# Kernel optimization log

Measured on AMD Instinct MI355X. Metric: run time of the kernel, lower is better.

## Reference

```python
import jax, jax.numpy as jnp
import numpy as np

D_MODEL = 512
H = 8


def setup_inputs() -> dict:
    key = jax.random.key(0)
    ks = jax.random.split(key, 11)
    B, L, D = 8, 1024, D_MODEL
    s = 1.0 / np.sqrt(D)
    return {
        "q": jax.random.normal(ks[0], (B, L, D), jnp.float32),
        "k": jax.random.normal(ks[1], (B, L, D), jnp.float32),
        "v": jax.random.normal(ks[2], (B, L, D), jnp.float32),
        "Wq": jax.random.normal(ks[3], (D, D), jnp.float32) * s,
        "bq": jnp.zeros((D,), jnp.float32),
        "Wk": jax.random.normal(ks[4], (D, D), jnp.float32) * s,
        "bk": jnp.zeros((D,), jnp.float32),
        "Wv": jax.random.normal(ks[5], (D, D), jnp.float32) * s,
        "bv": jnp.zeros((D,), jnp.float32),
        "Wo": jax.random.normal(ks[6], (D, D), jnp.float32) * s,
        "bo": jnp.zeros((D,), jnp.float32),
    }


def _split_heads(x, h):
    B, L, D = x.shape
    return x.reshape(B, L, h, D // h).transpose(0, 2, 1, 3)  # (B,h,L,dk)


def reference(q, k, v, Wq, bq, Wk, bk, Wv, bv, Wo, bo):
    B, L, D = q.shape
    dk = D // H
    qw = q @ Wq + bq
    kw = k @ Wk + bk
    vw = q @ Wv + bv  # faithful to source bug: dense_v applied to q, not v
    qh = _split_heads(qw, H)
    kh = _split_heads(kw, H)
    vh = _split_heads(vw, H)
    scale = jnp.asarray(1.0 / np.sqrt(dk), qh.dtype)
    scores = jnp.einsum("bhqd,bhkd->bhqk", qh, kh) * scale  # (B,h,L,L)
    attn = jax.nn.softmax(scores, axis=-1)
    ctx = jnp.einsum("bhqk,bhkd->bhqd", attn, vh)  # (B,h,L,dk)
    out = ctx.transpose(0, 2, 1, 3).reshape(B, L, D) @ Wo + bo
    return out, attn
```

## Files before the change

### kernel.cpp

```cpp
#include <hip/hip_runtime.h>

typedef unsigned short u16;
typedef __bf16 bf16x8 __attribute__((ext_vector_type(8)));
typedef unsigned short u16x8 __attribute__((ext_vector_type(8)));
typedef unsigned short u16x4 __attribute__((ext_vector_type(4)));
typedef float f32x4 __attribute__((ext_vector_type(4)));

#define MFMA16(a, b, c) __builtin_amdgcn_mfma_f32_16x16x32_bf16(a, b, c, 0, 0, 0)

__device__ __forceinline__ u16 f2bf(float f) {
    union { float f; unsigned u; } v; v.f = f;
    unsigned r = v.u + 0x7fffu + ((v.u >> 16) & 1u);
    return (u16)(r >> 16);
}
__device__ __forceinline__ float bf2f(u16 u) {
    union { unsigned u; float f; } v; v.u = (unsigned)u << 16;
    return v.f;
}
__device__ __forceinline__ u16 bfc(float f) {
    return __builtin_bit_cast(u16, (__bf16)f);
}

typedef __attribute__((address_space(1))) void GAS;
typedef __attribute__((address_space(3))) void LAS;
__device__ __forceinline__ void gload_lds16(const void* g, void* l) {
    __builtin_amdgcn_global_load_lds((GAS*)g, (LAS*)l, 16, 0, 0);
}

__global__ __launch_bounds__(256) void wtrans(const float* Wq, const float* Wk,
                                              const float* Wv, const float* Wo, u16* WT) {
    __shared__ float t[32][33];
    const int z = blockIdx.z;
    const float* W = (z == 0) ? Wq : (z == 1) ? Wk : (z == 2) ? Wv : Wo;
    u16* out = WT + (size_t)z * 512 * 512;
    const int tx = threadIdx.x, ty = threadIdx.y;
    const int k0 = blockIdx.y * 32, n0 = blockIdx.x * 32;
#pragma unroll
    for (int p = 0; p < 4; ++p)
        t[ty + 8 * p][tx] = W[(size_t)(k0 + ty + 8 * p) * 512 + n0 + tx];
    __syncthreads();
#pragma unroll
    for (int p = 0; p < 4; ++p) {
        const int n = n0 + ty + 8 * p;
        out[(size_t)n * 512 + k0 + tx] = f2bf(t[tx][ty + 8 * p]);
    }
}

__global__ __launch_bounds__(256) void qkconv(const float* q, const float* k, u16* qb, u16* kb) {
    const size_t n4 = (size_t)8192 * 512 / 4;
    const size_t stride = (size_t)gridDim.x * 256;
    for (size_t i = (size_t)blockIdx.x * 256 + threadIdx.x; i < 2 * n4; i += stride) {
        const float4 v = (i < n4) ? ((const float4*)q)[i] : ((const float4*)k)[i - n4];
        u16x4 o;
        o[0] = f2bf(v.x); o[1] = f2bf(v.y); o[2] = f2bf(v.z); o[3] = f2bf(v.w);
        if (i < n4) ((u16x4*)qb)[i] = o; else ((u16x4*)kb)[i - n4] = o;
    }
}

__global__ __launch_bounds__(256) void vtrans(const u16* vw, u16* vt) {
    __shared__ u16 t[64][72];
    const int l0 = blockIdx.x * 64, h = blockIdx.y, b = blockIdx.z;
    const int tid = threadIdx.x;
    {
        const int r = tid >> 2, c16 = (tid & 3) * 16;
        const u16* src = vw + (size_t)(b * 1024 + l0 + r) * 512 + h * 64 + c16;
        *(u16x8*)(&t[r][c16])     = *(const u16x8*)(src);
        *(u16x8*)(&t[r][c16 + 8]) = *(const u16x8*)(src + 8);
    }
    __syncthreads();
    {
        const int dk = tid >> 2, lc = (tid & 3) * 16;
        u16x8 a0, a1;
#pragma unroll
        for (int e = 0; e < 8; ++e) { a0[e] = t[lc + e][dk]; a1[e] = t[lc + 8 + e][dk]; }
        u16* dst = vt + ((size_t)(b * 8 + h) * 64 + dk) * 1024 + l0 + lc;
        *(u16x8*)dst       = a0;
        *(u16x8*)(dst + 8) = a1;
    }
}

template <bool C_F32>
__device__ __forceinline__ void gemm_core(const u16* A, const u16* Bt,
                                          const float* bias, void* Cp,
                                          int bm, int bn) {
    __shared__ u16 As[128 * 64];
    __shared__ u16 Bs[128 * 64];
    const int tid  = threadIdx.x;
    const int lane = tid & 63;
    const int w    = tid >> 6;
    const int wm   = (w >> 1) * 64;
    const int wn   = (w & 1) * 64;
    const int col  = lane & 15;
    const int quad = lane >> 4;
    const int srow = lane >> 3;
    const int scol = (lane & 7) * 8;

    f32x4 acc[4][4] = {};

    for (int kt = 0; kt < 512; kt += 64) {
        __syncthreads();
#pragma unroll
        for (int p = 0; p < 4; ++p) {
            const int c  = w * 4 + p;
            const int gr = c * 8 + srow;
            gload_lds16(A  + (size_t)(bm * 128 + gr) * 512 + kt + scol, As + c * 512);
            gload_lds16(Bt + (size_t)(bn * 128 + gr) * 512 + kt + scol, Bs + c * 512);
        }
        __syncthreads();
#pragma unroll
        for (int ks = 0; ks < 2; ++ks) {
            const int k0 = ks * 32 + quad * 8;
            bf16x8 af[4], bfr[4];
#pragma unroll
            for (int i = 0; i < 4; ++i)
                af[i] = __builtin_bit_cast(bf16x8, *(const u16x8*)(As + (wm + i * 16 + col) * 64 + k0));
#pragma unroll
            for (int j = 0; j < 4; ++j)
                bfr[j] = __builtin_bit_cast(bf16x8, *(const u16x8*)(Bs + (wn + j * 16 + col) * 64 + k0));
#pragma unroll
            for (int i = 0; i < 4; ++i)
#pragma unroll
                for (int j = 0; j < 4; ++j)
                    acc[i][j] = MFMA16(af[i], bfr[j], acc[i][j]);
        }
    }
#pragma unroll
    for (int j = 0; j < 4; ++j) {
        const int gn = bn * 128 + wn + j * 16 + col;
        const float bv = bias[gn];
#pragma unroll
        for (int i = 0; i < 4; ++i) {
#pragma unroll
            for (int r = 0; r < 4; ++r) {
                const int gm = bm * 128 + wm + i * 16 + quad * 4 + r;
                const float val = acc[i][j][r] + bv;
                if (C_F32) ((float*)Cp)[(size_t)gm * 512 + gn] = val;
                else       ((u16*)Cp)[(size_t)gm * 512 + gn]   = f2bf(val);
            }
        }
    }
}

__global__ __launch_bounds__(256, 3) void qkv_gemm(const u16* qb, const u16* kb, const u16* WT,
                                                   const float* bq, const float* bk, const float* bv,
                                                   u16* out) {
    const int z = blockIdx.z;
    const u16* A      = (z == 1) ? kb : qb;
    const u16* B      = WT + (size_t)z * 512 * 512;
    const float* bias = (z == 0) ? bq : (z == 1) ? bk : bv;
    u16* C            = out + (size_t)z * 8192 * 512;
    gemm_core<false>(A, B, bias, C, blockIdx.x, blockIdx.y);
}

__global__ __launch_bounds__(256, 3) void out_gemm(const u16* ctx, const u16* WoT,
                                                   const float* bo, float* out) {
    gemm_core<true>(ctx, WoT, bo, out, blockIdx.x, blockIdx.y);
}

__global__ __launch_bounds__(512, 4) void attn_kernel(const u16* qw, const u16* kw, const u16* vt,
                                                      float* attn_out, u16* ctx) {
    __shared__ u16 Ks[128 * 72];
    __shared__ u16 Vs[64 * 136];
    __shared__ u16 Ps[8][16 * 136];

    const int bh  = blockIdx.x;
    const int qt  = blockIdx.y;
    const int b   = bh >> 3, h = bh & 7;
    const int tid = threadIdx.x;
    const int lane = tid & 63, w = tid >> 6;
    const int col = lane & 15, quad = lane >> 4;
    const int wq  = w * 16;
    const float scale = 0.125f;

    const size_t headbase = (size_t)b * (1024 * 512) + (size_t)h * 64;
    const u16* vh = vt + (size_t)bh * (64 * 1024);

    const int krow = tid >> 2, koff = (tid & 3) * 16;
    const int vrow = tid >> 3, voff = (tid & 7) * 16;
    const u16* kbase = kw + headbase + (size_t)krow * 512 + koff;
    const u16* vbase = vh + (size_t)vrow * 1024 + voff;

    bf16x8 qf[2];
    {
        const u16* qp = qw + headbase + (size_t)(qt * 128 + wq + col) * 512 + quad * 8;
        qf[0] = __builtin_bit_cast(bf16x8, *(const u16x8*)qp);
        qf[1] = __builtin_bit_cast(bf16x8, *(const u16x8*)(qp + 32));
    }

    float l_acc = 0.f;

    u16x8 rk0 = *(const u16x8*)kbase;
    u16x8 rk1 = *(const u16x8*)(kbase + 8);
    for (int kt = 0; kt < 8; ++kt) {
        __syncthreads();
        *(u16x8*)(Ks + krow * 72 + koff)     = rk0;
        *(u16x8*)(Ks + krow * 72 + koff + 8) = rk1;
        __syncthreads();
        if (kt < 7) {
            const u16* kp = kbase + (size_t)(kt + 1) * (128 * 512);
            rk0 = *(const u16x8*)kp;
            rk1 = *(const u16x8*)(kp + 8);
        }
        f32x4 s[8] = {};
#pragma unroll
        for (int ks = 0; ks < 2; ++ks) {
            const int k0 = ks * 32 + quad * 8;
#pragma unroll
            for (int j = 0; j < 8; ++j) {
                const bf16x8 kf = __builtin_bit_cast(bf16x8,
                    *(const u16x8*)(Ks + (j * 16 + col) * 72 + k0));
                s[j] = MFMA16(kf, qf[ks], s[j]);
            }
        }
#pragma unroll
        for (int j = 0; j < 8; ++j)
#pragma unroll
            for (int r = 0; r < 4; ++r)
                l_acc += __expf(s[j][r] * scale);
    }

    float rinv;
    {
        float l = l_acc;
        l += __shfl_xor(l, 16); l += __shfl_xor(l, 32);
        rinv = 1.0f / l;
    }

    f32x4 o[4] = {};

    rk0 = *(const u16x8*)kbase;
    rk1 = *(const u16x8*)(kbase + 8);
    u16x8 rv0 = *(const u16x8*)vbase;
    u16x8 rv1 = *(const u16x8*)(vbase + 8);
    for (int kt = 0; kt < 8; ++kt) {
        __syncthreads();
        *(u16x8*)(Ks + krow * 72 + koff)      = rk0;
        *(u16x8*)(Ks + krow * 72 + koff + 8)  = rk1;
        *(u16x8*)(Vs + vrow * 136 + voff)     = rv0;
        *(u16x8*)(Vs + vrow * 136 + voff + 8) = rv1;
        __syncthreads();
        if (kt < 7) {
            const u16* kp = kbase + (size_t)(kt + 1) * (128 * 512);
            rk0 = *(const u16x8*)kp;
            rk1 = *(const u16x8*)(kp + 8);
            const u16* vp = vbase + (kt + 1) * 128;
            rv0 = *(const u16x8*)vp;
            rv1 = *(const u16x8*)(vp + 8);
        }
        u16* pw = &Ps[w][0];
#pragma unroll
        for (int half = 0; half < 2; ++half) {
            f32x4 s[4] = {};
#pragma unroll
            for (int ks = 0; ks < 2; ++ks) {
                const int k0 = ks * 32 + quad * 8;
#pragma unroll
                for (int j = 0; j < 4; ++j) {
                    const bf16x8 kf = __builtin_bit_cast(bf16x8,
                        *(const u16x8*)(Ks + (half * 64 + j * 16 + col) * 72 + k0));
                    s[j] = MFMA16(kf, qf[ks], s[j]);
                }
            }
#pragma unroll
            for (int j = 0; j < 4; ++j) {
                u16x4 pk;
                pk[0] = bfc(__expf(s[j][0] * scale) * rinv);
                pk[1] = bfc(__expf(s[j][1] * scale) * rinv);
                pk[2] = bfc(__expf(s[j][2] * scale) * rinv);
                pk[3] = bfc(__expf(s[j][3] * scale) * rinv);
                *(u16x4*)(pw + col * 136 + half * 64 + j * 16 + quad * 4) = pk;
            }
        }
        {
            const int r2 = lane >> 5;
            const int c0 = (lane & 31) * 4;
            float* ao = attn_out + ((size_t)bh * 1024 + (size_t)(qt * 128 + wq)) * 1024
                        + (size_t)kt * 128;
#pragma unroll
            for (int it = 0; it < 8; ++it) {
                const int row = it * 2 + r2;
                const u16x4 pv = *(const u16x4*)(pw + row * 136 + c0);
                f32x4 f;
                f[0] = bf2f(pv[0]); f[1] = bf2f(pv[1]); f[2] = bf2f(pv[2]); f[3] = bf2f(pv[3]);
                __builtin_nontemporal_store(f, (f32x4*)(ao + (size_t)row * 1024 + c0));
            }
        }
#pragma unroll
        for (int ks = 0; ks < 4; ++ks) {
            const int k0 = ks * 32 + quad * 8;
            const bf16x8 pf = __builtin_bit_cast(bf16x8, *(const u16x8*)(pw + col * 136 + k0));
#pragma unroll
            for (int j = 0; j < 4; ++j) {
                const bf16x8 vf = __builtin_bit_cast(bf16x8,
                    *(const u16x8*)(Vs + (j * 16 + col) * 136 + k0));
                o[j] = MFMA16(pf, vf, o[j]);
            }
        }
    }

#pragma unroll
    for (int j = 0; j < 4; ++j)
#pragma unroll
        for (int r = 0; r < 4; ++r) {
            const int qg = qt * 128 + wq + quad * 4 + r;
            ctx[(size_t)(b * 1024 + qg) * 512 + h * 64 + j * 16 + col] = f2bf(o[j][r]);
        }
}

extern "C" void kernel_launch(void* const* d_in, const int* in_sizes, int n_in,
                              void* d_out, int out_size, void* d_ws, size_t ws_size,
                              hipStream_t stream) {
    (void)in_sizes; (void)n_in; (void)out_size; (void)ws_size;
    const float* q  = (const float*)d_in[0];
    const float* k  = (const float*)d_in[1];
    const float* Wq = (const float*)d_in[3];
    const float* bq = (const float*)d_in[4];
    const float* Wk = (const float*)d_in[5];
    const float* bk = (const float*)d_in[6];
    const float* Wv = (const float*)d_in[7];
    const float* bv = (const float*)d_in[8];
    const float* Wo = (const float*)d_in[9];
    const float* bo = (const float*)d_in[10];

    float* out  = (float*)d_out;
    float* attn = (float*)d_out + (size_t)8 * 1024 * 512;

    char* ws = (char*)d_ws;
    u16* WT  = (u16*)ws;
    u16* qb  = (u16*)(ws + (size_t)2 * 1024 * 1024);
    u16* kb  = qb + (size_t)8192 * 512;
    u16* qkv = kb + (size_t)8192 * 512;
    u16* qw  = qkv;
    u16* kw  = qkv + (size_t)8192 * 512;
    u16* vw  = qkv + (size_t)2 * 8192 * 512;
    u16* ctx = qkv + (size_t)3 * 8192 * 512;
    u16* vt  = qkv + (size_t)4 * 8192 * 512;

    wtrans     <<<dim3(16, 16, 4), dim3(32, 8), 0, stream>>>(Wq, Wk, Wv, Wo, WT);
    qkconv     <<<dim3(2048),      256,          0, stream>>>(q, k, qb, kb);
    qkv_gemm   <<<dim3(64, 4, 3),  256,          0, stream>>>(qb, kb, WT, bq, bk, bv, qkv);
    vtrans     <<<dim3(16, 8, 8),  256,          0, stream>>>(vw, vt);
    attn_kernel<<<dim3(64, 8),     512,          0, stream>>>(qw, kw, vt, attn, ctx);
    out_gemm   <<<dim3(64, 4),     256,          0, stream>>>(ctx, WT + (size_t)3 * 512 * 512, bo, out);
}
```

Baseline: 410.6 us.

## Fuse V transpose into QKV GEMM epilogue and write attn probs directly

Drops the separate vtrans kernel: the V projection epilogue now writes bf16 results straight into the per-head transposed layout. In the attention kernel, fp32 probabilities go from registers to global memory, so the LDS readback, bf16-to-fp32 conversion and extra pass are gone. The attn output now keeps full fp32 precision. The cost is that attn stores become 16-byte fragments scattered across rows rather than coalesced row segments, and they lose the nontemporal hint.

```diff
diff --git a/kernel.cpp b/kernel.cpp
--- a/kernel.cpp
+++ b/kernel.cpp
@@ -57,29 +57,7 @@
     }
 }
 
-__global__ __launch_bounds__(256) void vtrans(const u16* vw, u16* vt) {
-    __shared__ u16 t[64][72];
-    const int l0 = blockIdx.x * 64, h = blockIdx.y, b = blockIdx.z;
-    const int tid = threadIdx.x;
-    {
-        const int r = tid >> 2, c16 = (tid & 3) * 16;
-        const u16* src = vw + (size_t)(b * 1024 + l0 + r) * 512 + h * 64 + c16;
-        *(u16x8*)(&t[r][c16])     = *(const u16x8*)(src);
-        *(u16x8*)(&t[r][c16 + 8]) = *(const u16x8*)(src + 8);
-    }
-    __syncthreads();
-    {
-        const int dk = tid >> 2, lc = (tid & 3) * 16;
-        u16x8 a0, a1;
-#pragma unroll
-        for (int e = 0; e < 8; ++e) { a0[e] = t[lc + e][dk]; a1[e] = t[lc + 8 + e][dk]; }
-        u16* dst = vt + ((size_t)(b * 8 + h) * 64 + dk) * 1024 + l0 + lc;
-        *(u16x8*)dst       = a0;
-        *(u16x8*)(dst + 8) = a1;
-    }
-}
-
-template <bool C_F32>
+template <int CMODE>
 __device__ __forceinline__ void gemm_core(const u16* A, const u16* Bt,
                                           const float* bias, void* Cp,
                                           int bm, int bn) {
@@ -130,12 +108,23 @@
         const float bv = bias[gn];
 #pragma unroll
         for (int i = 0; i < 4; ++i) {
-#pragma unroll
-            for (int r = 0; r < 4; ++r) {
-                const int gm = bm * 128 + wm + i * 16 + quad * 4 + r;
-                const float val = acc[i][j][r] + bv;
-                if (C_F32) ((float*)Cp)[(size_t)gm * 512 + gn] = val;
-                else       ((u16*)Cp)[(size_t)gm * 512 + gn]   = f2bf(val);
+            if (CMODE == 2) {
+                const int gm0 = bm * 128 + wm + i * 16 + quad * 4;
+                u16x4 pk;
+#pragma unroll
+                for (int r = 0; r < 4; ++r) pk[r] = f2bf(acc[i][j][r] + bv);
+                u16* dst = (u16*)Cp
+                    + ((size_t)((gm0 >> 10) * 8 + (gn >> 6)) * 64 + (gn & 63)) * 1024
+                    + (gm0 & 1023);
+                *(u16x4*)dst = pk;
+            } else {
+#pragma unroll
+                for (int r = 0; r < 4; ++r) {
+                    const int gm = bm * 128 + wm + i * 16 + quad * 4 + r;
+                    const float val = acc[i][j][r] + bv;
+                    if (CMODE == 1) ((float*)Cp)[(size_t)gm * 512 + gn] = val;
+                    else            ((u16*)Cp)[(size_t)gm * 512 + gn]   = f2bf(val);
+                }
             }
         }
     }
@@ -143,18 +132,20 @@
 
 __global__ __launch_bounds__(256, 3) void qkv_gemm(const u16* qb, const u16* kb, const u16* WT,
                                                    const float* bq, const float* bk, const float* bv,
-                                                   u16* out) {
+                                                   u16* qkw, u16* vt) {
     const int z = blockIdx.z;
-    const u16* A      = (z == 1) ? kb : qb;
-    const u16* B      = WT + (size_t)z * 512 * 512;
-    const float* bias = (z == 0) ? bq : (z == 1) ? bk : bv;
-    u16* C            = out + (size_t)z * 8192 * 512;
-    gemm_core<false>(A, B, bias, C, blockIdx.x, blockIdx.y);
+    const u16* B = WT + (size_t)z * 512 * 512;
+    if (z == 0)
+        gemm_core<0>(qb, B, bq, qkw, blockIdx.x, blockIdx.y);
+    else if (z == 1)
+        gemm_core<0>(kb, B, bk, qkw + (size_t)8192 * 512, blockIdx.x, blockIdx.y);
+    else
+        gemm_core<2>(qb, B, bv, vt, blockIdx.x, blockIdx.y);
 }
 
 __global__ __launch_bounds__(256, 3) void out_gemm(const u16* ctx, const u16* WoT,
                                                    const float* bo, float* out) {
-    gemm_core<true>(ctx, WoT, bo, out, blockIdx.x, blockIdx.y);
+    gemm_core<1>(ctx, WoT, bo, out, blockIdx.x, blockIdx.y);
 }
 
 __global__ __launch_bounds__(512, 4) void attn_kernel(const u16* qw, const u16* kw, const u16* vt,
@@ -180,6 +171,8 @@
     const u16* kbase = kw + headbase + (size_t)krow * 512 + koff;
     const u16* vbase = vh + (size_t)vrow * 1024 + voff;
 
+    float* arow = attn_out + ((size_t)bh * 1024 + (size_t)(qt * 128 + wq + col)) * 1024;
+
     bf16x8 qf[2];
     {
         const u16* qp = qw + headbase + (size_t)(qt * 128 + wq + col) * 512 + quad * 8;
@@ -248,6 +241,7 @@
             rv1 = *(const u16x8*)(vp + 8);
         }
         u16* pw = &Ps[w][0];
+        float* atile = arow + kt * 128;
 #pragma unroll
         for (int half = 0; half < 2; ++half) {
             f32x4 s[4] = {};
@@ -263,26 +257,15 @@
             }
 #pragma unroll
             for (int j = 0; j < 4; ++j) {
+                f32x4 pn;
+#pragma unroll
+                for (int r = 0; r < 4; ++r)
+                    pn[r] = __expf(s[j][r] * scale) * rinv;
+                *(f32x4*)(atile + half * 64 + j * 16 + quad * 4) = pn;
                 u16x4 pk;
-                pk[0] = bfc(__expf(s[j][0] * scale) * rinv);
-                pk[1] = bfc(__expf(s[j][1] * scale) * rinv);
-                pk[2] = bfc(__expf(s[j][2] * scale) * rinv);
-                pk[3] = bfc(__expf(s[j][3] * scale) * rinv);
+                pk[0] = bfc(pn[0]); pk[1] = bfc(pn[1]);
+                pk[2] = bfc(pn[2]); pk[3] = bfc(pn[3]);
                 *(u16x4*)(pw + col * 136 + half * 64 + j * 16 + quad * 4) = pk;
-            }
-        }
-        {
-            const int r2 = lane >> 5;
-            const int c0 = (lane & 31) * 4;
-            float* ao = attn_out + ((size_t)bh * 1024 + (size_t)(qt * 128 + wq)) * 1024
-                        + (size_t)kt * 128;
-#pragma unroll
-            for (int it = 0; it < 8; ++it) {
-                const int row = it * 2 + r2;
-                const u16x4 pv = *(const u16x4*)(pw + row * 136 + c0);
-                f32x4 f;
-                f[0] = bf2f(pv[0]); f[1] = bf2f(pv[1]); f[2] = bf2f(pv[2]); f[3] = bf2f(pv[3]);
-                __builtin_nontemporal_store(f, (f32x4*)(ao + (size_t)row * 1024 + c0));
             }
         }
 #pragma unroll
@@ -332,14 +315,12 @@
     u16* qkv = kb + (size_t)8192 * 512;
     u16* qw  = qkv;
     u16* kw  = qkv + (size_t)8192 * 512;
-    u16* vw  = qkv + (size_t)2 * 8192 * 512;
+    u16* vt  = qkv + (size_t)2 * 8192 * 512;
     u16* ctx = qkv + (size_t)3 * 8192 * 512;
-    u16* vt  = qkv + (size_t)4 * 8192 * 512;
 
     wtrans     <<<dim3(16, 16, 4), dim3(32, 8), 0, stream>>>(Wq, Wk, Wv, Wo, WT);
     qkconv     <<<dim3(2048),      256,          0, stream>>>(q, k, qb, kb);
-    qkv_gemm   <<<dim3(64, 4, 3),  256,          0, stream>>>(qb, kb, WT, bq, bk, bv, qkv);
-    vtrans     <<<dim3(16, 8, 8),  256,          0, stream>>>(vw, vt);
+    qkv_gemm   <<<dim3(64, 4, 3),  256,          0, stream>>>(qb, kb, WT, bq, bk, bv, qkv, vt);
     attn_kernel<<<dim3(64, 8),     512,          0, stream>>>(qw, kw, vt, attn, ctx);
     out_gemm   <<<dim3(64, 4),     256,          0, stream>>>(ctx, WT + (size_t)3 * 512 * 512, bo, out);
 }
```

New measurement: 412.8 us. No clear change (+0.5%).
